# Kernel optimization log

Measured on AMD Instinct MI355X. Metric: run time of the kernel, lower is better.

Reference implementation:

```python
import jax, jax.numpy as jnp
import numpy as np

U, V = 208, 176  # hard-coded DFT output shape from the original DFT2D
B, C, KH, KW = 32, 8, 3, 3


def dft2d(p):
    """Faithful vectorization of the original nested-loop DFT2D.
    dft[l, k] = (1/(M*N)) * sum_{m,n} p[m,n] * exp(-2j*pi*(k*m/V + l*n/U)),
    output shape (U, V) = (208, 176). Note the (intentionally) non-standard
    normalization axes, copied exactly from the source.
    """
    M, N = p.shape
    km = jnp.outer(jnp.arange(V), jnp.arange(M)).astype(jnp.float32)  # (V, M)
    ln = jnp.outer(jnp.arange(U), jnp.arange(N)).astype(jnp.float32)  # (U, N)
    E1 = jnp.exp(-2j * jnp.pi * km / V)  # (V, M) complex64
    E2 = jnp.exp(-2j * jnp.pi * ln / U)  # (U, N) complex64
    return jnp.einsum('km,mn,ln->lk', E1, p.astype(jnp.complex64), E2) / (M * N)


def setup_inputs() -> dict:
    key = jax.random.key(0)
    k1, k2 = jax.random.split(key)
    x = jax.random.normal(k1, (B, C, U, V), dtype=jnp.float32)
    kernel = jax.random.normal(k2, (KH, KW, 1, 1), dtype=jnp.float32)
    bias = jnp.zeros((1,), dtype=jnp.float32)
    return {"x": x, "kernel": kernel, "bias": bias}


def reference(x, kernel, bias):
    # Build the symmetric spatial kernel: [[k, flip_h(k)], [flip_w(k), flip_hw(k)]]
    k2 = kernel[::-1, :, :, :]
    k3 = kernel[:, ::-1, :, :]
    k4 = kernel[::-1, ::-1, :, :]
    sk = jnp.concatenate([jnp.concatenate([kernel, k2], axis=0),
                          jnp.concatenate([k3, k4], axis=0)], axis=1)  # (2KH, 2KW, 1, 1)
    sk2d = sk[:, :, 0, 0]  # tf.squeeze -> (2KH, 2KW)

    # k-space representation of the kernel and 50th-percentile binary mask
    fft_k = dft2d(sk2d)  # (208, 176) complex
    r = jnp.real(fft_k)
    thr = jnp.percentile(r, 50.0, method='nearest')  # tfp.stats.percentile default
    mask = (r > thr).astype(jnp.float32)  # (208, 176)

    # FFT of the image over its innermost two dims, mask in k-space, inverse FFT
    fft_x = jnp.fft.fft2(x)  # (B, C, 208, 176) complex64
    out = jnp.abs(jnp.fft.ifft2(fft_x * mask))  # bias unused on the test path
    return out
```

## Files before the change

kernel.cpp:

```cpp
#include <hip/hip_runtime.h>
#include <math.h>

#define UU 208
#define VV 176
#define NPIX (UU*VV)
#define MASKBLKS 143
#define ROWBLKS 1664

typedef __attribute__((ext_vector_type(2))) float v2f;
typedef __attribute__((ext_vector_type(4))) float v4f;
typedef __attribute__((ext_vector_type(2))) _Float16 h2;

__device__ __forceinline__ v2f mk2(float x, float y){ v2f r; r.x = x; r.y = y; return r; }
__device__ __forceinline__ v2f sp(float s){ v2f r; r.x = s; r.y = s; return r; }
__device__ __forceinline__ h2  toh(v2f a){ h2 r; r.x = (_Float16)a.x; r.y = (_Float16)a.y; return r; }
__device__ __forceinline__ v2f tof(h2 a){ return mk2((float)a.x, (float)a.y); }

template<bool INV>
__device__ __forceinline__ v2f cmulc(v2f a, float wx, float wy_fwd){
  const float wy = INV ? -wy_fwd : wy_fwd;
  return sp(a.x) * mk2(wx, wy) + sp(a.y) * mk2(-wy, wx);
}
__device__ __forceinline__ v2f cmulw4(v2f a, v4f t){
  return sp(a.x) * mk2(t.x, t.y) + sp(a.y) * mk2(t.z, t.w);
}
__device__ __forceinline__ v2f cmulw4i(v2f a, v4f t){
  return sp(a.x) * mk2(t.x, t.z) + sp(a.y) * mk2(t.y, t.w);
}

template<bool INV>
__device__ __forceinline__ void dft4(v2f& x0, v2f& x1, v2f& x2, v2f& x3){
  v2f s0 = x0 + x2, d0 = x0 - x2;
  v2f s1 = x1 + x3, d1 = x1 - x3;
  v2f jd1;
  if (INV){ jd1.x = -d1.y; jd1.y =  d1.x; }
  else    { jd1.x =  d1.y; jd1.y = -d1.x; }
  x0 = s0 + s1; x2 = s0 - s1;
  x1 = d0 + jd1; x3 = d0 - jd1;
}

template<bool INV>
__device__ __forceinline__ void fft16(v2f v[16]){
  dft4<INV>(v[0], v[4], v[8],  v[12]);
  dft4<INV>(v[1], v[5], v[9],  v[13]);
  dft4<INV>(v[2], v[6], v[10], v[14]);
  dft4<INV>(v[3], v[7], v[11], v[15]);
  const float C1 = 0.92387953251128674f;
  const float S1 = 0.38268343236508978f;
  const float R2 = 0.70710678118654752f;
  v[5]  = cmulc<INV>(v[5],  C1, -S1);
  v[9]  = cmulc<INV>(v[9],  R2, -R2);
  v[13] = cmulc<INV>(v[13], S1, -C1);
  v[6]  = cmulc<INV>(v[6],  R2, -R2);
  v[10] = cmulc<INV>(v[10], 0.f, -1.f);
  v[14] = cmulc<INV>(v[14], -R2, -R2);
  v[7]  = cmulc<INV>(v[7],  S1, -C1);
  v[11] = cmulc<INV>(v[11], -R2, -R2);
  v[15] = cmulc<INV>(v[15], -C1,  S1);
  dft4<INV>(v[0],  v[1],  v[2],  v[3]);
  dft4<INV>(v[4],  v[5],  v[6],  v[7]);
  dft4<INV>(v[8],  v[9],  v[10], v[11]);
  dft4<INV>(v[12], v[13], v[14], v[15]);
}

template<int N, bool INV>
__device__ __forceinline__ void dftN(const v2f* __restrict__ t, v2f* __restrict__ F,
                                     const v2f* __restrict__ cs){
  v2f a = t[0];
  #pragma unroll
  for (int n = 1; n < N; n++) a += t[n];
  F[0] = a;
  #pragma unroll
  for (int k = 1; k <= N/2; k++){
    v2f C = t[0], S = sp(0.f);
    #pragma unroll
    for (int n = 1; n < N; n++){
      const int idx = (n * k) % N;
      C += t[n] * sp(cs[idx].x);
      S += t[n] * sp(cs[idx].y);
    }
    v2f ssw; ssw.x = S.y; ssw.y = -S.x;
    if (!INV){ F[k] = C + ssw; F[N-k] = C - ssw; }
    else     { F[k] = C - ssw; F[N-k] = C + ssw; }
  }
}

__device__ __forceinline__ unsigned sortable(float f){
  unsigned u = __float_as_uint(f);
  return (u & 0x80000000u) ? ~u : (u | 0x80000000u);
}

template<int PER>
__device__ __forceinline__ unsigned findNk(const unsigned* __restrict__ bins_g,
                                           unsigned* sWS, unsigned* sRes, unsigned* kRef){
  const int t = threadIdx.x, lane = t & 63, wv = t >> 6;
  unsigned c[PER]; unsigned s = 0;
  #pragma unroll
  for (int j = 0; j < PER; j++){ c[j] = bins_g[t*PER + j]; s += c[j]; }
  unsigned v = s;
  #pragma unroll
  for (int d = 1; d < 64; d <<= 1){
    unsigned u = __shfl_up(v, d, 64);
    if (lane >= d) v += u;
  }
  if (lane == 63) sWS[wv] = v;
  __syncthreads();
  unsigned woff = 0;
  #pragma unroll
  for (int j = 0; j < 3; j++) woff += (j < wv) ? sWS[j] : 0u;
  unsigned incl = v + woff, excl = incl - s;
  unsigned k = *kRef;
  if (k >= excl && k < incl){
    unsigned kk = k - excl; unsigned b = (unsigned)(t*PER);
    #pragma unroll
    for (int j = 0; j < PER; j++){
      if (kk < c[j]){ b = (unsigned)(t*PER + j); break; }
      kk -= c[j];
    }
    sRes[0] = b; sRes[1] = kk;
  }
  __syncthreads();
  *kRef = sRes[1];
  unsigned b = sRes[0];
  __syncthreads();
  return b;
}

__device__ __forceinline__ float unsort(unsigned u){
  u = (u & 0x80000000u) ? (u ^ 0x80000000u) : ~u;
  return __uint_as_float(u);
}

__global__ __launch_bounds__(256) void rowfft_mask(const float* __restrict__ x, h2* __restrict__ freq,
                                                   const float* __restrict__ kin, float* __restrict__ rbuf,
                                                   unsigned* __restrict__ bins0){
  const double PI2 = 6.283185307179586476925286766559;
  __shared__ v4f wf[VV];
  __shared__ v2f cs11[11];
  __shared__ v2f mid[16][177];
  if (blockIdx.x >= ROWBLKS){
    unsigned* h = (unsigned*)&mid[0][0];
    int i = (blockIdx.x - ROWBLKS) * 256 + threadIdx.x;
    int l = i / VV, k = i - l * VV;
    double c1, s1, c2, s2;
    { double a = PI2 * (double)k / (double)VV; c1 = cos(a); s1 = sin(a); }
    { double a = PI2 * (double)l / (double)UU; c2 = cos(a); s2 = sin(a); }
    double cA[6], sA[6], cB[6], sB[6];
    cA[0] = 1.0; sA[0] = 0.0; cA[1] = c1; sA[1] = s1;
    cB[0] = 1.0; sB[0] = 0.0; cB[1] = c2; sB[1] = s2;
    #pragma unroll
    for (int m = 2; m < 6; m++){
      cA[m] = 2.0*c1*cA[m-1] - cA[m-2];
      sA[m] = 2.0*c1*sA[m-1] - sA[m-2];
      cB[m] = 2.0*c2*cB[m-1] - cB[m-2];
      sB[m] = 2.0*c2*sB[m-1] - sB[m-2];
    }
    const int rm[6] = {0, 1, 2, 2, 1, 0};
    double P[3], Q[3];
    #pragma unroll
    for (int a = 0; a < 3; a++){
      P[a] = 0.0; Q[a] = 0.0;
      #pragma unroll
      for (int n = 0; n < 6; n++){
        double kv = (double)kin[a*3 + rm[n]];
        P[a] += kv * cB[n];
        Q[a] += kv * sB[n];
      }
    }
    double s = 0.0;
    #pragma unroll
    for (int m = 0; m < 6; m++)
      s += cA[m]*P[rm[m]] - sA[m]*Q[rm[m]];
    float val = (float)(s / 36.0);
    rbuf[i] = val;
    const unsigned uval = sortable(val);
    #pragma unroll
    for (int j = 0; j < 8; j++) h[threadIdx.x*8 + j] = 0u;
    __syncthreads();
    atomicAdd(&h[uval >> 21], 1u);
    __syncthreads();
    #pragma unroll
    for (int j = 0; j < 8; j++){
      unsigned hv = h[threadIdx.x*8 + j];
      if (hv) atomicAdd(&bins0[threadIdx.x*8 + j], hv);
    }
    return;
  }
  { int i = threadIdx.x;
    if (i < VV){
      double a = -PI2 * (double)i / (double)VV;
      float c = (float)cos(a), s = (float)sin(a);
      v4f f; f.x = c; f.y = s; f.z = -s; f.w = c; wf[i] = f;
    }
    if (i < 11){
      double a = PI2 * (double)i / 11.0;
      cs11[i] = mk2((float)cos(a), (float)sin(a));
    } }
  const int gr = threadIdx.x >> 4, ln = threadIdx.x & 15;
  const int row = blockIdx.x * 16 + gr;
  const int p = row / UU, rr = row - p * UU;
  const float* xr1 = x + ((size_t)(2*p) * UU + rr) * VV;
  const float* xr2 = xr1 + (size_t)NPIX;
  h2* fr = freq + (size_t)row * VV;
  __syncthreads();
  if (ln < 11){
    v2f v[16];
    #pragma unroll
    for (int a = 0; a < 16; a++) v[a] = mk2(xr1[11*a + ln], xr2[11*a + ln]);
    fft16<false>(v);
    #pragma unroll
    for (int j = 0; j < 16; j++)
      mid[gr][j*11 + ln] = cmulw4(v[4*(j&3) + (j>>2)], wf[ln*j]);
  }
  v2f t[11], F[11];
  #pragma unroll
  for (int n2 = 0; n2 < 11; n2++) t[n2] = mid[gr][ln*11 + n2];
  dftN<11,false>(t, F, cs11);
  #pragma unroll
  for (int k2 = 0; k2 < 11; k2++) fr[ln + 16*k2] = toh(F[k2]);
}

__global__ __launch_bounds__(256) void hist1(const float* __restrict__ rbuf,
                                             const unsigned* __restrict__ bins0,
                                             unsigned* __restrict__ bins1){
  __shared__ unsigned h[2048];
  __shared__ unsigned sWS[4], sRes[2];
  #pragma unroll
  for (int j = 0; j < 8; j++) h[threadIdx.x*8 + j] = 0u;
  unsigned kk = 18304u;
  unsigned b0 = findNk<8>(bins0, sWS, sRes, &kk);
  int i = blockIdx.x * 256 + threadIdx.x;
  unsigned uval = sortable(rbuf[i]);
  if ((uval >> 21) == b0) atomicAdd(&h[(uval >> 10) & 2047u], 1u);
  __syncthreads();
  #pragma unroll
  for (int j = 0; j < 8; j++){
    unsigned hv = h[threadIdx.x*8 + j];
    if (hv) atomicAdd(&bins1[threadIdx.x*8 + j], hv);
  }
}

__global__ __launch_bounds__(256) void hist2(const float* __restrict__ rbuf,
                                             const unsigned* __restrict__ bins0,
                                             const unsigned* __restrict__ bins1,
                                             unsigned* __restrict__ bins2){
  __shared__ unsigned h[1024];
  __shared__ unsigned sWS[4], sRes[2];
  #pragma unroll
  for (int j = 0; j < 4; j++) h[threadIdx.x*4 + j] = 0u;
  unsigned kk = 18304u;
  unsigned b0 = findNk<8>(bins0, sWS, sRes, &kk);
  unsigned b1 = findNk<8>(bins1, sWS, sRes, &kk);
  int i = blockIdx.x * 256 + threadIdx.x;
  unsigned uval = sortable(rbuf[i]);
  if ((uval >> 10) == ((b0 << 11) | b1)) atomicAdd(&h[uval & 1023u], 1u);
  __syncthreads();
  #pragma unroll
  for (int j = 0; j < 4; j++){
    unsigned hv = h[threadIdx.x*4 + j];
    if (hv) atomicAdd(&bins2[threadIdx.x*4 + j], hv);
  }
}

__global__ __launch_bounds__(256) void colfft(h2* __restrict__ freq,
                                              const float* __restrict__ rbuf,
                                              const unsigned* __restrict__ bins0,
                                              const unsigned* __restrict__ bins1,
                                              const unsigned* __restrict__ bins2){
  __shared__ v4f wf[UU];
  __shared__ v2f cs13[13];
  __shared__ v2f buf[UU*17];
  __shared__ unsigned sWS[4], sRes[2];
  { int i = threadIdx.x;
    const double PI2 = 6.283185307179586476925286766559;
    if (i < UU){
      double a = -PI2 * (double)i / (double)UU;
      float c = (float)cos(a), s = (float)sin(a);
      v4f f; f.x = c; f.y = s; f.z = -s; f.w = c; wf[i] = f;
    }
    if (i < 13){
      double a = PI2 * (double)i / 13.0;
      cs13[i] = mk2((float)cos(a), (float)sin(a));
    } }
  unsigned kk = 18304u;
  unsigned b0 = findNk<8>(bins0, sWS, sRes, &kk);
  unsigned b1 = findNk<8>(bins1, sWS, sRes, &kk);
  unsigned b2 = findNk<4>(bins2, sWS, sRes, &kk);
  const float thr = unsort((b0 << 21) | (b1 << 10) | b2);
  const int role = threadIdx.x >> 4, c = threadIdx.x & 15;
  const int img = blockIdx.x / 11;
  const int v0 = (blockIdx.x - img*11) << 4;
  h2* base = freq + (size_t)img * NPIX + v0 + c;
  __syncthreads();
  if (role < 13){
    v2f v[16];
    #pragma unroll
    for (int a = 0; a < 16; a++) v[a] = tof(base[(13*a + role)*VV]);
    fft16<false>(v);
    #pragma unroll
    for (int j = 0; j < 16; j++)
      buf[(j*13 + role)*17 + c] = cmulw4(v[4*(j&3) + (j>>2)], wf[role*j]);
  }
  __syncthreads();
  v2f F[13];
  {
    v2f t[13];
    #pragma unroll
    for (int n2 = 0; n2 < 13; n2++) t[n2] = buf[(role*13 + n2)*17 + c];
    dftN<13,false>(t, F, cs13);
    #pragma unroll
    for (int k2 = 0; k2 < 13; k2++){
      int u = role + 16*k2;
      float m = (rbuf[u*VV + v0 + c] > thr) ? 1.0f : 0.0f;
      F[k2] *= sp(m);
    }
  }
  __syncthreads();
  #pragma unroll
  for (int k2 = 0; k2 < 13; k2++) buf[(role + 16*k2)*17 + c] = F[k2];
  __syncthreads();
  if (role < 13){
    v2f v[16];
    #pragma unroll
    for (int a = 0; a < 16; a++) v[a] = buf[(13*a + role)*17 + c];
    fft16<true>(v);
    #pragma unroll
    for (int j = 0; j < 16; j++)
      buf[(j*13 + role)*17 + c] = cmulw4i(v[4*(j&3) + (j>>2)], wf[role*j]);
  }
  __syncthreads();
  {
    v2f t[13], G[13];
    #pragma unroll
    for (int n2 = 0; n2 < 13; n2++) t[n2] = buf[(role*13 + n2)*17 + c];
    dftN<13,true>(t, G, cs13);
    #pragma unroll
    for (int k2 = 0; k2 < 13; k2++)
      base[(role + 16*k2)*VV] = toh(G[k2]);
  }
}

__global__ __launch_bounds__(256) void rowifft_abs(const h2* __restrict__ freq, float* __restrict__ out){
  __shared__ v4f wf[VV];
  __shared__ v2f cs11[11];
  __shared__ v2f mid[16][177];
  { int i = threadIdx.x;
    const double PI2 = 6.283185307179586476925286766559;
    if (i < VV){
      double a = -PI2 * (double)i / (double)VV;
      float c = (float)cos(a), s = (float)sin(a);
      v4f f; f.x = c; f.y = s; f.z = -s; f.w = c; wf[i] = f;
    }
    if (i < 11){
      double a = PI2 * (double)i / 11.0;
      cs11[i] = mk2((float)cos(a), (float)sin(a));
    } }
  const int gr = threadIdx.x >> 4, ln = threadIdx.x & 15;
  const int row = blockIdx.x * 16 + gr;
  const int p = row / UU, rr = row - p * UU;
  const h2* fr = freq + (size_t)row * VV;
  float* orow1 = out + ((size_t)(2*p) * UU + rr) * VV;
  float* orow2 = orow1 + (size_t)NPIX;
  __syncthreads();
  if (ln < 11){
    v2f v[16];
    #pragma unroll
    for (int a = 0; a < 16; a++) v[a] = tof(fr[11*a + ln]);
    fft16<true>(v);
    #pragma unroll
    for (int j = 0; j < 16; j++)
      mid[gr][j*11 + ln] = cmulw4i(v[4*(j&3) + (j>>2)], wf[ln*j]);
  }
  v2f t[11], G[11];
  #pragma unroll
  for (int n2 = 0; n2 < 11; n2++) t[n2] = mid[gr][ln*11 + n2];
  dftN<11,true>(t, G, cs11);
  #pragma unroll
  for (int k2 = 0; k2 < 11; k2++){
    orow1[ln + 16*k2] = fabsf(G[k2].x) * (1.0f / 36608.0f);
    orow2[ln + 16*k2] = fabsf(G[k2].y) * (1.0f / 36608.0f);
  }
}

extern "C" void kernel_launch(void* const* d_in, const int* in_sizes, int n_in,
                              void* d_out, int out_size, void* d_ws, size_t ws_size,
                              hipStream_t stream){
  const float* x   = (const float*)d_in[0];
  const float* kin = (const float*)d_in[1];
  float* out = (float*)d_out;
  char* ws = (char*)d_ws;
  h2*       freq  = (h2*)ws;
  float*    rbuf  = (float*)(ws + 18743296);
  unsigned* bins0 = (unsigned*)(ws + 18889728);
  unsigned* bins1 = bins0 + 2048;
  unsigned* bins2 = bins1 + 2048;

  hipMemsetAsync(bins0, 0, (2048 + 2048 + 1024) * 4, stream);
  hipLaunchKernelGGL(rowfft_mask, dim3(ROWBLKS + MASKBLKS), dim3(256), 0, stream,
                     x, freq, kin, rbuf, bins0);
  hipLaunchKernelGGL(hist1,       dim3(143),  dim3(256), 0, stream, rbuf, bins0, bins1);
  hipLaunchKernelGGL(hist2,       dim3(143),  dim3(256), 0, stream, rbuf, bins0, bins1, bins2);
  hipLaunchKernelGGL(colfft,      dim3(1408), dim3(256), 0, stream, freq, rbuf, bins0, bins1, bins2);
  hipLaunchKernelGGL(rowifft_abs, dim3(1664), dim3(256), 0, stream, freq, out);
}
```

Baseline: 78.11 us.

## Store intermediate spectrum in fp32 and precompute threshold in a single-block kernel

Switches the intermediate frequency buffer from half-precision to fp32 complex, which doubles the traffic through the row and column FFT passes but removes conversion work and fp16 precision loss. It also moves the three-level percentile search out of every colfft block into a dedicated one-block kernel that writes the threshold to workspace, adding one launch. The mask values are prefetched into registers before the twiddle setup so their loads can overlap.

```diff
diff --git a/kernel.cpp b/kernel.cpp
--- a/kernel.cpp
+++ b/kernel.cpp
@@ -9,12 +9,9 @@
 
 typedef __attribute__((ext_vector_type(2))) float v2f;
 typedef __attribute__((ext_vector_type(4))) float v4f;
-typedef __attribute__((ext_vector_type(2))) _Float16 h2;
 
 __device__ __forceinline__ v2f mk2(float x, float y){ v2f r; r.x = x; r.y = y; return r; }
 __device__ __forceinline__ v2f sp(float s){ v2f r; r.x = s; r.y = s; return r; }
-__device__ __forceinline__ h2  toh(v2f a){ h2 r; r.x = (_Float16)a.x; r.y = (_Float16)a.y; return r; }
-__device__ __forceinline__ v2f tof(h2 a){ return mk2((float)a.x, (float)a.y); }
 
 template<bool INV>
 __device__ __forceinline__ v2f cmulc(v2f a, float wx, float wy_fwd){
@@ -126,12 +123,7 @@
   return b;
 }
 
-__device__ __forceinline__ float unsort(unsigned u){
-  u = (u & 0x80000000u) ? (u ^ 0x80000000u) : ~u;
-  return __uint_as_float(u);
-}
-
-__global__ __launch_bounds__(256) void rowfft_mask(const float* __restrict__ x, h2* __restrict__ freq,
+__global__ __launch_bounds__(256) void rowfft_mask(const float* __restrict__ x, v2f* __restrict__ freq,
                                                    const float* __restrict__ kin, float* __restrict__ rbuf,
                                                    unsigned* __restrict__ bins0){
   const double PI2 = 6.283185307179586476925286766559;
@@ -201,7 +193,7 @@
   const int p = row / UU, rr = row - p * UU;
   const float* xr1 = x + ((size_t)(2*p) * UU + rr) * VV;
   const float* xr2 = xr1 + (size_t)NPIX;
-  h2* fr = freq + (size_t)row * VV;
+  v2f* fr = freq + (size_t)row * VV;
   __syncthreads();
   if (ln < 11){
     v2f v[16];
@@ -217,7 +209,7 @@
   for (int n2 = 0; n2 < 11; n2++) t[n2] = mid[gr][ln*11 + n2];
   dftN<11,false>(t, F, cs11);
   #pragma unroll
-  for (int k2 = 0; k2 < 11; k2++) fr[ln + 16*k2] = toh(F[k2]);
+  for (int k2 = 0; k2 < 11; k2++) fr[ln + 16*k2] = F[k2];
 }
 
 __global__ __launch_bounds__(256) void hist1(const float* __restrict__ rbuf,
@@ -262,40 +254,52 @@
   }
 }
 
-__global__ __launch_bounds__(256) void colfft(h2* __restrict__ freq,
-                                              const float* __restrict__ rbuf,
-                                              const unsigned* __restrict__ bins0,
-                                              const unsigned* __restrict__ bins1,
-                                              const unsigned* __restrict__ bins2){
+__global__ __launch_bounds__(256) void thr_final(const unsigned* __restrict__ bins0,
+                                                 const unsigned* __restrict__ bins1,
+                                                 const unsigned* __restrict__ bins2,
+                                                 float* __restrict__ thrOut){
+  __shared__ unsigned sWS[4], sRes[2];
+  unsigned kk = 18304u;
+  unsigned b0 = findNk<8>(bins0, sWS, sRes, &kk);
+  unsigned b1 = findNk<8>(bins1, sWS, sRes, &kk);
+  unsigned b2 = findNk<4>(bins2, sWS, sRes, &kk);
+  if (threadIdx.x == 0){
+    unsigned u = (b0 << 21) | (b1 << 10) | b2;
+    u = (u & 0x80000000u) ? (u ^ 0x80000000u) : ~u;
+    thrOut[0] = __uint_as_float(u);
+  }
+}
+
+__global__ __launch_bounds__(256) void colfft(v2f* __restrict__ freq,
+                                              const float* __restrict__ rbuf, const float* __restrict__ thrp){
   __shared__ v4f wf[UU];
   __shared__ v2f cs13[13];
   __shared__ v2f buf[UU*17];
-  __shared__ unsigned sWS[4], sRes[2];
+  const int role = threadIdx.x >> 4, c = threadIdx.x & 15;
+  const int img = blockIdx.x / 11;
+  const int v0 = (blockIdx.x - img*11) << 4;
+  v2f* base = freq + (size_t)img * NPIX + v0 + c;
+  const float thr = thrp[0];
+  float mv[13];
+  #pragma unroll
+  for (int k2 = 0; k2 < 13; k2++)
+    mv[k2] = rbuf[(role + 16*k2)*VV + v0 + c];
   { int i = threadIdx.x;
     const double PI2 = 6.283185307179586476925286766559;
     if (i < UU){
       double a = -PI2 * (double)i / (double)UU;
-      float c = (float)cos(a), s = (float)sin(a);
-      v4f f; f.x = c; f.y = s; f.z = -s; f.w = c; wf[i] = f;
+      float cc = (float)cos(a), ss = (float)sin(a);
+      v4f f; f.x = cc; f.y = ss; f.z = -ss; f.w = cc; wf[i] = f;
     }
     if (i < 13){
       double a = PI2 * (double)i / 13.0;
       cs13[i] = mk2((float)cos(a), (float)sin(a));
     } }
-  unsigned kk = 18304u;
-  unsigned b0 = findNk<8>(bins0, sWS, sRes, &kk);
-  unsigned b1 = findNk<8>(bins1, sWS, sRes, &kk);
-  unsigned b2 = findNk<4>(bins2, sWS, sRes, &kk);
-  const float thr = unsort((b0 << 21) | (b1 << 10) | b2);
-  const int role = threadIdx.x >> 4, c = threadIdx.x & 15;
-  const int img = blockIdx.x / 11;
-  const int v0 = (blockIdx.x - img*11) << 4;
-  h2* base = freq + (size_t)img * NPIX + v0 + c;
   __syncthreads();
   if (role < 13){
     v2f v[16];
     #pragma unroll
-    for (int a = 0; a < 16; a++) v[a] = tof(base[(13*a + role)*VV]);
+    for (int a = 0; a < 16; a++) v[a] = base[(13*a + role)*VV];
     fft16<false>(v);
     #pragma unroll
     for (int j = 0; j < 16; j++)
@@ -310,8 +314,7 @@
     dftN<13,false>(t, F, cs13);
     #pragma unroll
     for (int k2 = 0; k2 < 13; k2++){
-      int u = role + 16*k2;
-      float m = (rbuf[u*VV + v0 + c] > thr) ? 1.0f : 0.0f;
+      float m = (mv[k2] > thr) ? 1.0f : 0.0f;
       F[k2] *= sp(m);
     }
   }
@@ -336,11 +339,11 @@
     dftN<13,true>(t, G, cs13);
     #pragma unroll
     for (int k2 = 0; k2 < 13; k2++)
-      base[(role + 16*k2)*VV] = toh(G[k2]);
-  }
-}
-
-__global__ __launch_bounds__(256) void rowifft_abs(const h2* __restrict__ freq, float* __restrict__ out){
+      base[(role + 16*k2)*VV] = G[k2];
+  }
+}
+
+__global__ __launch_bounds__(256) void rowifft_abs(const v2f* __restrict__ freq, float* __restrict__ out){
   __shared__ v4f wf[VV];
   __shared__ v2f cs11[11];
   __shared__ v2f mid[16][177];
@@ -358,14 +361,14 @@
   const int gr = threadIdx.x >> 4, ln = threadIdx.x & 15;
   const int row = blockIdx.x * 16 + gr;
   const int p = row / UU, rr = row - p * UU;
-  const h2* fr = freq + (size_t)row * VV;
+  const v2f* fr = freq + (size_t)row * VV;
   float* orow1 = out + ((size_t)(2*p) * UU + rr) * VV;
   float* orow2 = orow1 + (size_t)NPIX;
   __syncthreads();
   if (ln < 11){
     v2f v[16];
     #pragma unroll
-    for (int a = 0; a < 16; a++) v[a] = tof(fr[11*a + ln]);
+    for (int a = 0; a < 16; a++) v[a] = fr[11*a + ln];
     fft16<true>(v);
     #pragma unroll
     for (int j = 0; j < 16; j++)
@@ -389,9 +392,10 @@
   const float* kin = (const float*)d_in[1];
   float* out = (float*)d_out;
   char* ws = (char*)d_ws;
-  h2*       freq  = (h2*)ws;
-  float*    rbuf  = (float*)(ws + 18743296);
-  unsigned* bins0 = (unsigned*)(ws + 18889728);
+  v2f*      freq  = (v2f*)ws;
+  float*    rbuf  = (float*)(ws + 37486592);
+  float*    thr   = (float*)(ws + 37633024);
+  unsigned* bins0 = (unsigned*)(ws + 37633040);
   unsigned* bins1 = bins0 + 2048;
   unsigned* bins2 = bins1 + 2048;
 
@@ -400,6 +404,7 @@
                      x, freq, kin, rbuf, bins0);
   hipLaunchKernelGGL(hist1,       dim3(143),  dim3(256), 0, stream, rbuf, bins0, bins1);
   hipLaunchKernelGGL(hist2,       dim3(143),  dim3(256), 0, stream, rbuf, bins0, bins1, bins2);
-  hipLaunchKernelGGL(colfft,      dim3(1408), dim3(256), 0, stream, freq, rbuf, bins0, bins1, bins2);
+  hipLaunchKernelGGL(thr_final,   dim3(1),    dim3(256), 0, stream, bins0, bins1, bins2, thr);
+  hipLaunchKernelGGL(colfft,      dim3(1408), dim3(256), 0, stream, freq, rbuf, thr);
   hipLaunchKernelGGL(rowifft_abs, dim3(1664), dim3(256), 0, stream, freq, out);
 }
```

Measured after the change: 78.03 us. No clear change (-0.1%).
